# Performance work log

Hardware: AMD Instinct MI355X
Metric: run time of the kernel (lower is better)

Reference implementation:

```python
import jax, jax.numpy as jnp
import numpy as np

N_GENES = 20000
HIDDEN = 64
K_HOPS = 2
N_EDGES = 640000
BATCH = 32
BN_EPS = 1e-5


def setup_inputs() -> dict:
    key = jax.random.key(0)
    ks = jax.random.split(key, 8)
    B, N, d, E = BATCH, N_GENES, HIDDEN, N_EDGES
    x = jax.random.normal(ks[0], (B, N), jnp.float32)
    edge_index = jax.random.randint(ks[1], (2, E), 0, N).astype(jnp.int64)
    gene_emb = jax.random.normal(ks[2], (N, d), jnp.float32) * 0.02
    W_sg = jax.random.normal(ks[3], (d, d), jnp.float32) / np.sqrt(d).astype(np.float32)
    b_sg = jnp.zeros((d,), jnp.float32)
    W1 = jax.random.normal(ks[4], (d, 2 * d), jnp.float32) / np.sqrt(d).astype(np.float32)
    b1 = jnp.zeros((2 * d,), jnp.float32)
    gamma1 = jnp.ones((2 * d,), jnp.float32)
    beta1 = jnp.zeros((2 * d,), jnp.float32)
    W2 = jax.random.normal(ks[5], (2 * d, 1), jnp.float32) / np.sqrt(2 * d).astype(np.float32)
    b2 = jnp.zeros((1,), jnp.float32)
    return dict(x=x, edge_index=edge_index, gene_emb=gene_emb, W_sg=W_sg, b_sg=b_sg,
                W1=W1, b1=b1, gamma1=gamma1, beta1=beta1, W2=W2, b2=b2)


def _sgconv(gene_emb, src, dst, W_sg, b_sg):
    # SGConv: h = (D^{-1/2}(A+I)D^{-1/2})^K X W  on the co-expression graph
    N = gene_emb.shape[0]
    ones = jnp.ones(src.shape, gene_emb.dtype)
    deg = jax.ops.segment_sum(ones, dst, num_segments=N) + 1.0  # +1 self loop
    dinv = jax.lax.rsqrt(deg)
    ew = dinv[src] * dinv[dst]          # [E] symmetric edge norm
    self_w = (dinv * dinv)[:, None]     # [N,1] self-loop weight
    h = gene_emb
    for _ in range(K_HOPS):
        msg = h[src] * ew[:, None]      # gather + scale  [E,d]
        h = jax.ops.segment_sum(msg, dst, num_segments=N) + h * self_w
    return h @ W_sg + b_sg              # [N,d]


def reference(x, edge_index, gene_emb, W_sg, b_sg, W1, b1, gamma1, beta1, W2, b2):
    B, N = x.shape
    src, dst = edge_index[0], edge_index[1]
    h = _sgconv(gene_emb, src, dst, W_sg, b_sg)         # [N,d]
    # per-(cell, gene) state: expression scales the gene's graph embedding
    z = (x[:, :, None] * h[None, :, :]).reshape(B * N, -1)  # [B*N, d]
    # MLP block: Linear -> BatchNorm1d (train-mode batch stats) -> ReLU -> Linear
    z = z @ W1 + b1                                     # [B*N, 2d]
    mu = jnp.mean(z, axis=0)
    var = jnp.var(z, axis=0)
    z = (z - mu) * jax.lax.rsqrt(var + BN_EPS) * gamma1 + beta1
    z = jax.nn.relu(z)
    delta = (z @ W2 + b2).reshape(B, N)                 # per-gene scalar delta
    return x + delta                                    # residual post-perturbation expression
```

## Files before the change

### kernel.cpp

```cpp
#include <hip/hip_runtime.h>
#include <hip/hip_bf16.h>

#define NG 20000
#define HD 64
#define NE 640000
#define NB 32
#define D2 128
#define BN_EPS 1e-5f
#define BSTRIDE 128

__device__ __forceinline__ unsigned pack_bf16(float x, float y) {
    unsigned ux = __float_as_uint(x), uy = __float_as_uint(y);
    unsigned lo = (ux + 0x7FFFu + ((ux >> 16) & 1u)) >> 16;
    unsigned hi = (uy + 0x7FFFu + ((uy >> 16) & 1u)) >> 16;
    return (hi << 16) | lo;
}
__device__ __forceinline__ float2 unpack_bf16(unsigned g) {
    return make_float2(__uint_as_float(g << 16), __uint_as_float(g & 0xFFFF0000u));
}


__global__ void k_scatter(const int* __restrict__ src, const int* __restrict__ dst,
                          int* __restrict__ cnt, int* __restrict__ srcs) {
    int e4 = blockIdx.x * blockDim.x + threadIdx.x;
    int4 s = ((const int4*)src)[e4];
    int4 d = ((const int4*)dst)[e4];
    srcs[(d.x << 7) + atomicAdd(&cnt[d.x], 1)] = s.x;
    srcs[(d.y << 7) + atomicAdd(&cnt[d.y], 1)] = s.y;
    srcs[(d.z << 7) + atomicAdd(&cnt[d.z], 1)] = s.z;
    srcs[(d.w << 7) + atomicAdd(&cnt[d.w], 1)] = s.w;
}

#define MB_COL 79
#define MB_WC  33
#define MB_PRE 625

__global__ __launch_bounds__(256) void k_misc(const float* __restrict__ x,
                                              const float* __restrict__ W_sg,
                                              const float* __restrict__ b_sg,
                                              const float* __restrict__ W1,
                                              const float* __restrict__ emb,
                                              const int* __restrict__ cnt,
                                              float* __restrict__ sx,
                                              float* __restrict__ sxx,
                                              float* __restrict__ S,
                                              float* __restrict__ Wc,
                                              float* __restrict__ bc,
                                              unsigned* __restrict__ g0) {
    int blk = blockIdx.x;
    int tid = threadIdx.x;
    if (blk < MB_COL) {
        if (blk == 0 && tid < 2 * D2) S[tid] = 0.f;
        int n = blk * 256 + tid;
        if (n < NG) {
            float s = 0.f, s2 = 0.f;
            #pragma unroll
            for (int b = 0; b < NB; ++b) {
                float v = x[b * NG + n];
                s += v;
                s2 = fmaf(v, v, s2);
            }
            sx[n] = s;
            sxx[n] = s2;
        }
    } else if (blk < MB_COL + MB_WC) {
        int idx = (blk - MB_COL) * 256 + tid;
        if (idx < HD * D2) {
            int k = idx >> 7, c = idx & (D2 - 1);
            float acc = 0.f;
            #pragma unroll 8
            for (int j = 0; j < HD; ++j) acc += W_sg[k * HD + j] * W1[j * D2 + c];
            Wc[idx] = acc;
        } else if (idx < HD * D2 + D2) {
            int c = idx - HD * D2;
            float acc = 0.f;
            #pragma unroll 8
            for (int j = 0; j < HD; ++j) acc += b_sg[j] * W1[j * D2 + c];
            bc[c] = acc;
        }
    } else {
        int i = (blk - MB_COL - MB_WC) * 256 + tid;
        int row = i >> 3;
        float dv = rsqrtf((float)cnt[row] + 1.0f);
        float4 a = ((const float4*)emb)[i * 2];
        float4 b = ((const float4*)emb)[i * 2 + 1];
        uint4 o;
        o.x = pack_bf16(a.x * dv, a.y * dv);
        o.y = pack_bf16(a.z * dv, a.w * dv);
        o.z = pack_bf16(b.x * dv, b.y * dv);
        o.w = pack_bf16(b.z * dv, b.w * dv);
        ((uint4*)g0)[i] = o;
    }
}

template<bool SQ>
__global__ __launch_bounds__(256) void k_gather(const int* __restrict__ srcs,
                                                const int* __restrict__ cnt,
                                                const unsigned* __restrict__ g,
                                                unsigned* __restrict__ outb,
                                                float4* __restrict__ outf) {
    int n = blockIdx.x * 16 + (threadIdx.x >> 4);
    int l = threadIdx.x & 15;
    const uint2* gp = (const uint2*)g + l;
    int len = cnt[n];
    const int* row = srcs + (n << 7);
    uint2 sv = gp[n * 16];
    float2 a0 = unpack_bf16(sv.x), a1 = unpack_bf16(sv.y);
    float ax = a0.x, ay = a0.y, az = a1.x, aw = a1.y;
    int j = 0;
    for (; j + 3 < len; j += 4) {
        int s0 = row[j], s1 = row[j + 1], s2 = row[j + 2], s3 = row[j + 3];
        uint2 v0 = gp[s0 * 16], v1 = gp[s1 * 16], v2 = gp[s2 * 16], v3 = gp[s3 * 16];
        float2 x0 = unpack_bf16(v0.x), y0 = unpack_bf16(v0.y);
        float2 x1 = unpack_bf16(v1.x), y1 = unpack_bf16(v1.y);
        float2 x2 = unpack_bf16(v2.x), y2 = unpack_bf16(v2.y);
        float2 x3 = unpack_bf16(v3.x), y3 = unpack_bf16(v3.y);
        ax += (x0.x + x1.x) + (x2.x + x3.x);
        ay += (x0.y + x1.y) + (x2.y + x3.y);
        az += (y0.x + y1.x) + (y2.x + y3.x);
        aw += (y0.y + y1.y) + (y2.y + y3.y);
    }
    for (; j < len; ++j) {
        uint2 v0 = gp[row[j] * 16];
        float2 x0 = unpack_bf16(v0.x), y0 = unpack_bf16(v0.y);
        ax += x0.x; ay += x0.y; az += y0.x; aw += y0.y;
    }
    float dv = rsqrtf((float)len + 1.0f);
    float sc = SQ ? dv * dv : dv;
    ax *= sc; ay *= sc; az *= sc; aw *= sc;
    if (SQ) {
        uint2 o;
        o.x = pack_bf16(ax, ay);
        o.y = pack_bf16(az, aw);
        ((uint2*)outb)[n * 16 + l] = o;
    } else {
        outf[n * 16 + l] = make_float4(ax, ay, az, aw);
    }
}

#define PR 32

__global__ __launch_bounds__(256) void k_p_stats(const float* __restrict__ h2,
                                                 const float* __restrict__ Wc,
                                                 const float* __restrict__ bc,
                                                 const float* __restrict__ sx,
                                                 const float* __restrict__ sxx,
                                                 float* __restrict__ p,
                                                 float* __restrict__ S) {
    __shared__ float lWc[HD * D2];
    __shared__ float lt[HD * PR];
    __shared__ float lsx[PR], lsxx[PR];
    int tid = threadIdx.x;
    int n0 = blockIdx.x * PR;

    for (int i = tid; i < HD * D2 / 4; i += 256)
        ((float4*)lWc)[i] = ((const float4*)Wc)[i];
    {
        int r = tid & 31, kb = tid >> 5;
        #pragma unroll
        for (int pp = 0; pp < 2; ++pp) {
            int k4 = kb + pp * 8;
            float4 v = ((const float4*)(h2 + (size_t)(n0 + r) * HD))[k4];
            lt[(k4 * 4 + 0) * PR + r] = v.x;
            lt[(k4 * 4 + 1) * PR + r] = v.y;
            lt[(k4 * 4 + 2) * PR + r] = v.z;
            lt[(k4 * 4 + 3) * PR + r] = v.w;
        }
        if (tid < PR) { lsx[tid] = sx[n0 + tid]; lsxx[tid] = sxx[n0 + tid]; }
    }
    __syncthreads();

    int cg = tid & 31;
    int rg = tid >> 5;
    float acc[4][4];
    #pragma unroll
    for (int i = 0; i < 4; ++i)
        #pragma unroll
        for (int j = 0; j < 4; ++j) acc[i][j] = 0.f;

    #pragma unroll 4
    for (int k = 0; k < HD; ++k) {
        float4 wv = *(const float4*)&lWc[k * D2 + cg * 4];
        float4 hv = *(const float4*)&lt[k * PR + rg * 4];
        acc[0][0] = fmaf(hv.x, wv.x, acc[0][0]);
        acc[0][1] = fmaf(hv.x, wv.y, acc[0][1]);
        acc[0][2] = fmaf(hv.x, wv.z, acc[0][2]);
        acc[0][3] = fmaf(hv.x, wv.w, acc[0][3]);
        acc[1][0] = fmaf(hv.y, wv.x, acc[1][0]);
        acc[1][1] = fmaf(hv.y, wv.y, acc[1][1]);
        acc[1][2] = fmaf(hv.y, wv.z, acc[1][2]);
        acc[1][3] = fmaf(hv.y, wv.w, acc[1][3]);
        acc[2][0] = fmaf(hv.z, wv.x, acc[2][0]);
        acc[2][1] = fmaf(hv.z, wv.y, acc[2][1]);
        acc[2][2] = fmaf(hv.z, wv.z, acc[2][2]);
        acc[2][3] = fmaf(hv.z, wv.w, acc[2][3]);
        acc[3][0] = fmaf(hv.w, wv.x, acc[3][0]);
        acc[3][1] = fmaf(hv.w, wv.y, acc[3][1]);
        acc[3][2] = fmaf(hv.w, wv.z, acc[3][2]);
        acc[3][3] = fmaf(hv.w, wv.w, acc[3][3]);
    }

    float4 bcv = ((const float4*)bc)[cg];
    float s1[4] = {0.f, 0.f, 0.f, 0.f};
    float s2[4] = {0.f, 0.f, 0.f, 0.f};
    #pragma unroll
    for (int i = 0; i < 4; ++i) {
        int rr = rg * 4 + i;
        float xs = lsx[rr], xss = lsxx[rr];
        float4 o;
        o.x = acc[i][0] + bcv.x;
        o.y = acc[i][1] + bcv.y;
        o.z = acc[i][2] + bcv.z;
        o.w = acc[i][3] + bcv.w;
        s1[0] = fmaf(o.x, xs, s1[0]);  s2[0] = fmaf(o.x * o.x, xss, s2[0]);
        s1[1] = fmaf(o.y, xs, s1[1]);  s2[1] = fmaf(o.y * o.y, xss, s2[1]);
        s1[2] = fmaf(o.z, xs, s1[2]);  s2[2] = fmaf(o.z * o.z, xss, s2[2]);
        s1[3] = fmaf(o.w, xs, s1[3]);  s2[3] = fmaf(o.w * o.w, xss, s2[3]);
        ((float4*)(p + (size_t)(n0 + rr) * D2))[cg] = o;
    }

    __syncthreads();
    *(float4*)&lt[rg * D2 + cg * 4]        = make_float4(s1[0], s1[1], s1[2], s1[3]);
    *(float4*)&lt[1024 + rg * D2 + cg * 4] = make_float4(s2[0], s2[1], s2[2], s2[3]);
    __syncthreads();
    if (tid < D2) {
        float a = 0.f, b = 0.f;
        #pragma unroll
        for (int g2 = 0; g2 < 8; ++g2) {
            a += lt[g2 * D2 + tid];
            b += lt[1024 + g2 * D2 + tid];
        }
        atomicAdd(&S[tid], a);
        atomicAdd(&S[D2 + tid], b);
    }
}

#define FN 64

__global__ __launch_bounds__(256) void k_final(const float* __restrict__ x,
                                               const float* __restrict__ p,
                                               const float* __restrict__ S,
                                               const float* __restrict__ gamma1,
                                               const float* __restrict__ beta1,
                                               const float* __restrict__ W2,
                                               const float* __restrict__ b2,
                                               float* __restrict__ out) {
    __shared__ float lp[FN * 129];
    __shared__ float ls[D2], lo[D2], lw[D2];
    int tid = threadIdx.x;
    int n0 = blockIdx.x * FN;
    if (tid < D2) {
        const float inv = 1.0f / (float)(NB * NG);
        float m1 = S[tid] * inv;
        float m2 = S[D2 + tid] * inv;
        float a = gamma1[tid] * rsqrtf(m2 - m1 * m1 + BN_EPS);
        ls[tid] = a;
        lo[tid] = beta1[tid] - m1 * a;
        lw[tid] = W2[tid];
    }
    for (int i = tid; i < FN * D2 / 4; i += 256) {
        int row = i >> 5, c4 = i & 31;
        int n = n0 + row;
        float4 v = (n < NG) ? ((const float4*)(p + n * D2))[c4]
                            : make_float4(0.f, 0.f, 0.f, 0.f);
        float* dp = lp + row * 129 + c4 * 4;
        dp[0] = v.x; dp[1] = v.y; dp[2] = v.z; dp[3] = v.w;
    }
    __syncthreads();
    int nl = tid & 63;
    int n = n0 + nl;
    if (n >= NG) return;
    int bbase = (tid >> 6) * 8;
    const float* prow = lp + nl * 129;
    float b2v = b2[0];
    float xv[8], acc[8];
    #pragma unroll
    for (int bi = 0; bi < 8; ++bi) {
        xv[bi] = x[(bbase + bi) * NG + n];
        acc[bi] = 0.f;
    }
    #pragma unroll 8
    for (int c = 0; c < D2; ++c) {
        float ps = prow[c] * ls[c];
        float ocv = lo[c];
        float wv = lw[c];
        #pragma unroll
        for (int bi = 0; bi < 8; ++bi) {
            float v = fmaxf(fmaf(xv[bi], ps, ocv), 0.f);
            acc[bi] = fmaf(v, wv, acc[bi]);
        }
    }
    #pragma unroll
    for (int bi = 0; bi < 8; ++bi)
        out[(bbase + bi) * NG + n] = xv[bi] + acc[bi] + b2v;
}

extern "C" void kernel_launch(void* const* d_in, const int* in_sizes, int n_in,
                              void* d_out, int out_size, void* d_ws, size_t ws_size,
                              hipStream_t stream) {
    const float* x        = (const float*)d_in[0];
    const int*   ei       = (const int*)d_in[1];
    const float* gene_emb = (const float*)d_in[2];
    const float* W_sg     = (const float*)d_in[3];
    const float* b_sg     = (const float*)d_in[4];
    const float* W1       = (const float*)d_in[5];
    const float* gamma1   = (const float*)d_in[7];
    const float* beta1    = (const float*)d_in[8];
    const float* W2       = (const float*)d_in[9];
    const float* b2       = (const float*)d_in[10];
    float* out = (float*)d_out;

    const int* src = ei;
    const int* dst = ei + NE;

    char* base = (char*)d_ws;
    int*      srcs     = (int*)base;
    int*      cnt      = srcs + NG * BSTRIDE;
    unsigned* g0       = (unsigned*)(cnt + NG);
    unsigned* g1       = g0 + NG * 32;
    float*    h2       = (float*)(g1 + NG * 32);
    float*    Wc       = h2 + NG * HD;
    float*    bc       = Wc + HD * D2;
    float*    p        = bc + D2;
    float*    sx       = p + NG * D2;
    float*    sxx      = sx + NG;
    float*    S        = sxx + NG;

    hipMemsetAsync(cnt, 0, NG * sizeof(int), stream);

    k_scatter<<<NE / 4 / 256, 256, 0, stream>>>(src, dst, cnt, srcs);

    k_misc<<<MB_COL + MB_WC + MB_PRE, 256, 0, stream>>>(x, W_sg, b_sg, W1, gene_emb,
                                                        cnt, sx, sxx, S, Wc, bc, g0);

    k_gather<true><<<NG / 16, 256, 0, stream>>>(srcs, cnt, g0, g1, nullptr);
    k_gather<false><<<NG / 16, 256, 0, stream>>>(srcs, cnt, g1, nullptr, (float4*)h2);

    k_p_stats<<<NG / PR, 256, 0, stream>>>(h2, Wc, bc, sx, sxx, p, S);

    k_final<<<(NG + FN - 1) / FN, 256, 0, stream>>>(x, p, S, gamma1, beta1, W2, b2, out);
}
```

Baseline: 186.6 us.

## Fuse hop-2 gather into projection kernel, use 16-bit neighbor indices and wider gathers

Merges the second aggregation hop into the projection/statistics kernel so h2 is never written to or read back from global memory. Neighbor lists are stored as 16-bit indices, which halves the bucket footprint and lets eight indices load in one vector read. Gathers now move 16-byte rows using 8 lanes per node. The hipMemset is replaced by zeroing inside an init kernel, and the emb prescale step is split into its own launch that runs after the scatter. The 16-bit indices only work because N < 65536, and fewer lanes per node lowers parallelism on each neighbor list.

```diff
diff --git a/kernel.cpp b/kernel.cpp
--- a/kernel.cpp
+++ b/kernel.cpp
@@ -7,7 +7,6 @@
 #define NB 32
 #define D2 128
 #define BN_EPS 1e-5f
-#define BSTRIDE 128
 
 __device__ __forceinline__ unsigned pack_bf16(float x, float y) {
     unsigned ux = __float_as_uint(x), uy = __float_as_uint(y);
@@ -19,39 +18,34 @@
     return make_float2(__uint_as_float(g << 16), __uint_as_float(g & 0xFFFF0000u));
 }
 
-
-__global__ void k_scatter(const int* __restrict__ src, const int* __restrict__ dst,
-                          int* __restrict__ cnt, int* __restrict__ srcs) {
-    int e4 = blockIdx.x * blockDim.x + threadIdx.x;
-    int4 s = ((const int4*)src)[e4];
-    int4 d = ((const int4*)dst)[e4];
-    srcs[(d.x << 7) + atomicAdd(&cnt[d.x], 1)] = s.x;
-    srcs[(d.y << 7) + atomicAdd(&cnt[d.y], 1)] = s.y;
-    srcs[(d.z << 7) + atomicAdd(&cnt[d.z], 1)] = s.z;
-    srcs[(d.w << 7) + atomicAdd(&cnt[d.w], 1)] = s.w;
-}
-
-#define MB_COL 79
-#define MB_WC  33
-#define MB_PRE 625
-
-__global__ __launch_bounds__(256) void k_misc(const float* __restrict__ x,
+__device__ __forceinline__ void acc8(uint4 v, float& a0, float& a1, float& a2, float& a3,
+                                     float& a4, float& a5, float& a6, float& a7) {
+    float2 t0 = unpack_bf16(v.x), t1 = unpack_bf16(v.y);
+    float2 t2 = unpack_bf16(v.z), t3 = unpack_bf16(v.w);
+    a0 += t0.x; a1 += t0.y; a2 += t1.x; a3 += t1.y;
+    a4 += t2.x; a5 += t2.y; a6 += t3.x; a7 += t3.y;
+}
+
+#define IB_ZC 20
+#define IB_S  1
+#define IB_COL 79
+#define IB_WC 33
+
+__global__ __launch_bounds__(256) void k_init(const float* __restrict__ x,
                                               const float* __restrict__ W_sg,
                                               const float* __restrict__ b_sg,
                                               const float* __restrict__ W1,
-                                              const float* __restrict__ emb,
-                                              const int* __restrict__ cnt,
-                                              float* __restrict__ sx,
-                                              float* __restrict__ sxx,
-                                              float* __restrict__ S,
-                                              float* __restrict__ Wc,
-                                              float* __restrict__ bc,
-                                              unsigned* __restrict__ g0) {
-    int blk = blockIdx.x;
-    int tid = threadIdx.x;
-    if (blk < MB_COL) {
-        if (blk == 0 && tid < 2 * D2) S[tid] = 0.f;
-        int n = blk * 256 + tid;
+                                              int* __restrict__ cnt, float* __restrict__ S,
+                                              float* __restrict__ sx, float* __restrict__ sxx,
+                                              float* __restrict__ Wc, float* __restrict__ bc) {
+    int blk = blockIdx.x, tid = threadIdx.x;
+    if (blk < IB_ZC) {
+        int i = blk * 256 + tid;
+        if (i < NG / 4) ((int4*)cnt)[i] = make_int4(0, 0, 0, 0);
+    } else if (blk < IB_ZC + IB_S) {
+        S[tid] = 0.f;
+    } else if (blk < IB_ZC + IB_S + IB_COL) {
+        int n = (blk - IB_ZC - IB_S) * 256 + tid;
         if (n < NG) {
             float s = 0.f, s2 = 0.f;
             #pragma unroll
@@ -63,8 +57,8 @@
             sx[n] = s;
             sxx[n] = s2;
         }
-    } else if (blk < MB_COL + MB_WC) {
-        int idx = (blk - MB_COL) * 256 + tid;
+    } else {
+        int idx = (blk - IB_ZC - IB_S - IB_COL) * 256 + tid;
         if (idx < HD * D2) {
             int k = idx >> 7, c = idx & (D2 - 1);
             float acc = 0.f;
@@ -78,95 +72,151 @@
             for (int j = 0; j < HD; ++j) acc += b_sg[j] * W1[j * D2 + c];
             bc[c] = acc;
         }
-    } else {
-        int i = (blk - MB_COL - MB_WC) * 256 + tid;
-        int row = i >> 3;
-        float dv = rsqrtf((float)cnt[row] + 1.0f);
-        float4 a = ((const float4*)emb)[i * 2];
-        float4 b = ((const float4*)emb)[i * 2 + 1];
-        uint4 o;
-        o.x = pack_bf16(a.x * dv, a.y * dv);
-        o.y = pack_bf16(a.z * dv, a.w * dv);
-        o.z = pack_bf16(b.x * dv, b.y * dv);
-        o.w = pack_bf16(b.z * dv, b.w * dv);
-        ((uint4*)g0)[i] = o;
-    }
-}
-
-template<bool SQ>
-__global__ __launch_bounds__(256) void k_gather(const int* __restrict__ srcs,
+    }
+}
+
+
+__global__ void k_scatter(const int* __restrict__ src, const int* __restrict__ dst,
+                          int* __restrict__ cnt, unsigned short* __restrict__ srcs) {
+    int e4 = blockIdx.x * blockDim.x + threadIdx.x;
+    int4 s = ((const int4*)src)[e4];
+    int4 d = ((const int4*)dst)[e4];
+    srcs[(d.x << 7) + atomicAdd(&cnt[d.x], 1)] = (unsigned short)s.x;
+    srcs[(d.y << 7) + atomicAdd(&cnt[d.y], 1)] = (unsigned short)s.y;
+    srcs[(d.z << 7) + atomicAdd(&cnt[d.z], 1)] = (unsigned short)s.z;
+    srcs[(d.w << 7) + atomicAdd(&cnt[d.w], 1)] = (unsigned short)s.w;
+}
+
+
+__global__ __launch_bounds__(256) void k_pre(const float* __restrict__ emb,
+                                             const int* __restrict__ cnt,
+                                             unsigned* __restrict__ g0) {
+    int i = blockIdx.x * blockDim.x + threadIdx.x;
+    float dv = rsqrtf((float)cnt[i >> 3] + 1.0f);
+    float4 a = ((const float4*)emb)[i * 2];
+    float4 b = ((const float4*)emb)[i * 2 + 1];
+    uint4 o;
+    o.x = pack_bf16(a.x * dv, a.y * dv);
+    o.y = pack_bf16(a.z * dv, a.w * dv);
+    o.z = pack_bf16(b.x * dv, b.y * dv);
+    o.w = pack_bf16(b.z * dv, b.w * dv);
+    ((uint4*)g0)[i] = o;
+}
+
+
+__global__ __launch_bounds__(256) void k_gather1(const unsigned short* __restrict__ srcs,
+                                                 const int* __restrict__ cnt,
+                                                 const unsigned* __restrict__ g,
+                                                 unsigned* __restrict__ outb) {
+    int n = blockIdx.x * 32 + (threadIdx.x >> 3);
+    int l = threadIdx.x & 7;
+    const uint4* gp = (const uint4*)g + l;
+    int len = cnt[n];
+    const unsigned short* row = srcs + ((size_t)n << 7);
+    uint4 sv = gp[(size_t)n * 8];
+    float a0, a1, a2, a3, a4, a5, a6, a7;
+    {
+        float2 t0 = unpack_bf16(sv.x), t1 = unpack_bf16(sv.y);
+        float2 t2 = unpack_bf16(sv.z), t3 = unpack_bf16(sv.w);
+        a0 = t0.x; a1 = t0.y; a2 = t1.x; a3 = t1.y;
+        a4 = t2.x; a5 = t2.y; a6 = t3.x; a7 = t3.y;
+    }
+    int j = 0;
+    for (; j + 8 <= len; j += 8) {
+        uint4 iw = *(const uint4*)(row + j);
+        int i0 = iw.x & 0xFFFF, i1 = iw.x >> 16, i2 = iw.y & 0xFFFF, i3 = iw.y >> 16;
+        int i4 = iw.z & 0xFFFF, i5 = iw.z >> 16, i6 = iw.w & 0xFFFF, i7 = iw.w >> 16;
+        uint4 v0 = gp[(size_t)i0 * 8], v1 = gp[(size_t)i1 * 8];
+        uint4 v2 = gp[(size_t)i2 * 8], v3 = gp[(size_t)i3 * 8];
+        uint4 v4 = gp[(size_t)i4 * 8], v5 = gp[(size_t)i5 * 8];
+        uint4 v6 = gp[(size_t)i6 * 8], v7 = gp[(size_t)i7 * 8];
+        acc8(v0, a0, a1, a2, a3, a4, a5, a6, a7);
+        acc8(v1, a0, a1, a2, a3, a4, a5, a6, a7);
+        acc8(v2, a0, a1, a2, a3, a4, a5, a6, a7);
+        acc8(v3, a0, a1, a2, a3, a4, a5, a6, a7);
+        acc8(v4, a0, a1, a2, a3, a4, a5, a6, a7);
+        acc8(v5, a0, a1, a2, a3, a4, a5, a6, a7);
+        acc8(v6, a0, a1, a2, a3, a4, a5, a6, a7);
+        acc8(v7, a0, a1, a2, a3, a4, a5, a6, a7);
+    }
+    for (; j < len; ++j) {
+        uint4 v = gp[(size_t)row[j] * 8];
+        acc8(v, a0, a1, a2, a3, a4, a5, a6, a7);
+    }
+    float dv = rsqrtf((float)len + 1.0f);
+    float sc = dv * dv;
+    uint4 o;
+    o.x = pack_bf16(a0 * sc, a1 * sc);
+    o.y = pack_bf16(a2 * sc, a3 * sc);
+    o.z = pack_bf16(a4 * sc, a5 * sc);
+    o.w = pack_bf16(a6 * sc, a7 * sc);
+    ((uint4*)outb)[(size_t)n * 8 + l] = o;
+}
+
+
+__global__ __launch_bounds__(256) void k_hop2ps(const unsigned short* __restrict__ srcs,
                                                 const int* __restrict__ cnt,
                                                 const unsigned* __restrict__ g,
-                                                unsigned* __restrict__ outb,
-                                                float4* __restrict__ outf) {
-    int n = blockIdx.x * 16 + (threadIdx.x >> 4);
-    int l = threadIdx.x & 15;
-    const uint2* gp = (const uint2*)g + l;
-    int len = cnt[n];
-    const int* row = srcs + (n << 7);
-    uint2 sv = gp[n * 16];
-    float2 a0 = unpack_bf16(sv.x), a1 = unpack_bf16(sv.y);
-    float ax = a0.x, ay = a0.y, az = a1.x, aw = a1.y;
-    int j = 0;
-    for (; j + 3 < len; j += 4) {
-        int s0 = row[j], s1 = row[j + 1], s2 = row[j + 2], s3 = row[j + 3];
-        uint2 v0 = gp[s0 * 16], v1 = gp[s1 * 16], v2 = gp[s2 * 16], v3 = gp[s3 * 16];
-        float2 x0 = unpack_bf16(v0.x), y0 = unpack_bf16(v0.y);
-        float2 x1 = unpack_bf16(v1.x), y1 = unpack_bf16(v1.y);
-        float2 x2 = unpack_bf16(v2.x), y2 = unpack_bf16(v2.y);
-        float2 x3 = unpack_bf16(v3.x), y3 = unpack_bf16(v3.y);
-        ax += (x0.x + x1.x) + (x2.x + x3.x);
-        ay += (x0.y + x1.y) + (x2.y + x3.y);
-        az += (y0.x + y1.x) + (y2.x + y3.x);
-        aw += (y0.y + y1.y) + (y2.y + y3.y);
-    }
-    for (; j < len; ++j) {
-        uint2 v0 = gp[row[j] * 16];
-        float2 x0 = unpack_bf16(v0.x), y0 = unpack_bf16(v0.y);
-        ax += x0.x; ay += x0.y; az += y0.x; aw += y0.y;
-    }
-    float dv = rsqrtf((float)len + 1.0f);
-    float sc = SQ ? dv * dv : dv;
-    ax *= sc; ay *= sc; az *= sc; aw *= sc;
-    if (SQ) {
-        uint2 o;
-        o.x = pack_bf16(ax, ay);
-        o.y = pack_bf16(az, aw);
-        ((uint2*)outb)[n * 16 + l] = o;
-    } else {
-        outf[n * 16 + l] = make_float4(ax, ay, az, aw);
-    }
-}
-
-#define PR 32
-
-__global__ __launch_bounds__(256) void k_p_stats(const float* __restrict__ h2,
-                                                 const float* __restrict__ Wc,
-                                                 const float* __restrict__ bc,
-                                                 const float* __restrict__ sx,
-                                                 const float* __restrict__ sxx,
-                                                 float* __restrict__ p,
-                                                 float* __restrict__ S) {
+                                                const float* __restrict__ Wc,
+                                                const float* __restrict__ bc,
+                                                const float* __restrict__ sx,
+                                                const float* __restrict__ sxx,
+                                                float* __restrict__ p,
+                                                float* __restrict__ S) {
     __shared__ float lWc[HD * D2];
-    __shared__ float lt[HD * PR];
-    __shared__ float lsx[PR], lsxx[PR];
+    __shared__ float lt[HD * 32];
     int tid = threadIdx.x;
-    int n0 = blockIdx.x * PR;
+    int n0 = blockIdx.x * 32;
 
     for (int i = tid; i < HD * D2 / 4; i += 256)
         ((float4*)lWc)[i] = ((const float4*)Wc)[i];
+
     {
-        int r = tid & 31, kb = tid >> 5;
-        #pragma unroll
-        for (int pp = 0; pp < 2; ++pp) {
-            int k4 = kb + pp * 8;
-            float4 v = ((const float4*)(h2 + (size_t)(n0 + r) * HD))[k4];
-            lt[(k4 * 4 + 0) * PR + r] = v.x;
-            lt[(k4 * 4 + 1) * PR + r] = v.y;
-            lt[(k4 * 4 + 2) * PR + r] = v.z;
-            lt[(k4 * 4 + 3) * PR + r] = v.w;
-        }
-        if (tid < PR) { lsx[tid] = sx[n0 + tid]; lsxx[tid] = sxx[n0 + tid]; }
+        int r = tid >> 3, l = tid & 7;
+        int n = n0 + r;
+        const uint4* gp = (const uint4*)g + l;
+        int len = cnt[n];
+        const unsigned short* row = srcs + ((size_t)n << 7);
+        uint4 sv = gp[(size_t)n * 8];
+        float a0, a1, a2, a3, a4, a5, a6, a7;
+        {
+            float2 t0 = unpack_bf16(sv.x), t1 = unpack_bf16(sv.y);
+            float2 t2 = unpack_bf16(sv.z), t3 = unpack_bf16(sv.w);
+            a0 = t0.x; a1 = t0.y; a2 = t1.x; a3 = t1.y;
+            a4 = t2.x; a5 = t2.y; a6 = t3.x; a7 = t3.y;
+        }
+        int j = 0;
+        for (; j + 8 <= len; j += 8) {
+            uint4 iw = *(const uint4*)(row + j);
+            int i0 = iw.x & 0xFFFF, i1 = iw.x >> 16, i2 = iw.y & 0xFFFF, i3 = iw.y >> 16;
+            int i4 = iw.z & 0xFFFF, i5 = iw.z >> 16, i6 = iw.w & 0xFFFF, i7 = iw.w >> 16;
+            uint4 v0 = gp[(size_t)i0 * 8], v1 = gp[(size_t)i1 * 8];
+            uint4 v2 = gp[(size_t)i2 * 8], v3 = gp[(size_t)i3 * 8];
+            uint4 v4 = gp[(size_t)i4 * 8], v5 = gp[(size_t)i5 * 8];
+            uint4 v6 = gp[(size_t)i6 * 8], v7 = gp[(size_t)i7 * 8];
+            acc8(v0, a0, a1, a2, a3, a4, a5, a6, a7);
+            acc8(v1, a0, a1, a2, a3, a4, a5, a6, a7);
+            acc8(v2, a0, a1, a2, a3, a4, a5, a6, a7);
+            acc8(v3, a0, a1, a2, a3, a4, a5, a6, a7);
+            acc8(v4, a0, a1, a2, a3, a4, a5, a6, a7);
+            acc8(v5, a0, a1, a2, a3, a4, a5, a6, a7);
+            acc8(v6, a0, a1, a2, a3, a4, a5, a6, a7);
+            acc8(v7, a0, a1, a2, a3, a4, a5, a6, a7);
+        }
+        for (; j < len; ++j) {
+            uint4 v = gp[(size_t)row[j] * 8];
+            acc8(v, a0, a1, a2, a3, a4, a5, a6, a7);
+        }
+        float dv = rsqrtf((float)len + 1.0f);
+        int kb = l * 8;
+        lt[(kb + 0) * 32 + r] = a0 * dv;
+        lt[(kb + 1) * 32 + r] = a1 * dv;
+        lt[(kb + 2) * 32 + r] = a2 * dv;
+        lt[(kb + 3) * 32 + r] = a3 * dv;
+        lt[(kb + 4) * 32 + r] = a4 * dv;
+        lt[(kb + 5) * 32 + r] = a5 * dv;
+        lt[(kb + 6) * 32 + r] = a6 * dv;
+        lt[(kb + 7) * 32 + r] = a7 * dv;
     }
     __syncthreads();
 
@@ -181,7 +231,7 @@
     #pragma unroll 4
     for (int k = 0; k < HD; ++k) {
         float4 wv = *(const float4*)&lWc[k * D2 + cg * 4];
-        float4 hv = *(const float4*)&lt[k * PR + rg * 4];
+        float4 hv = *(const float4*)&lt[k * 32 + rg * 4];
         acc[0][0] = fmaf(hv.x, wv.x, acc[0][0]);
         acc[0][1] = fmaf(hv.x, wv.y, acc[0][1]);
         acc[0][2] = fmaf(hv.x, wv.z, acc[0][2]);
@@ -206,7 +256,7 @@
     #pragma unroll
     for (int i = 0; i < 4; ++i) {
         int rr = rg * 4 + i;
-        float xs = lsx[rr], xss = lsxx[rr];
+        float xs = sx[n0 + rr], xss = sxx[n0 + rr];
         float4 o;
         o.x = acc[i][0] + bcv.x;
         o.y = acc[i][1] + bcv.y;
@@ -261,7 +311,7 @@
     for (int i = tid; i < FN * D2 / 4; i += 256) {
         int row = i >> 5, c4 = i & 31;
         int n = n0 + row;
-        float4 v = (n < NG) ? ((const float4*)(p + n * D2))[c4]
+        float4 v = (n < NG) ? ((const float4*)(p + (size_t)n * D2))[c4]
                             : make_float4(0.f, 0.f, 0.f, 0.f);
         float* dp = lp + row * 129 + c4 * 4;
         dp[0] = v.x; dp[1] = v.y; dp[2] = v.z; dp[3] = v.w;
@@ -314,29 +364,24 @@
     const int* dst = ei + NE;
 
     char* base = (char*)d_ws;
-    int*      srcs     = (int*)base;
-    int*      cnt      = srcs + NG * BSTRIDE;
+    unsigned short* srcs = (unsigned short*)base;
+    int*      cnt      = (int*)(base + (size_t)NG * 128 * 2);
     unsigned* g0       = (unsigned*)(cnt + NG);
     unsigned* g1       = g0 + NG * 32;
-    float*    h2       = (float*)(g1 + NG * 32);
-    float*    Wc       = h2 + NG * HD;
+    float*    Wc       = (float*)(g1 + NG * 32);
     float*    bc       = Wc + HD * D2;
     float*    p        = bc + D2;
-    float*    sx       = p + NG * D2;
+    float*    sx       = p + (size_t)NG * D2;
     float*    sxx      = sx + NG;
     float*    S        = sxx + NG;
 
-    hipMemsetAsync(cnt, 0, NG * sizeof(int), stream);
-
+    k_init<<<IB_ZC + IB_S + IB_COL + IB_WC, 256, 0, stream>>>(x, W_sg, b_sg, W1,
+                                                              cnt, S, sx, sxx, Wc, bc);
     k_scatter<<<NE / 4 / 256, 256, 0, stream>>>(src, dst, cnt, srcs);
-
-    k_misc<<<MB_COL + MB_WC + MB_PRE, 256, 0, stream>>>(x, W_sg, b_sg, W1, gene_emb,
-                                                        cnt, sx, sxx, S, Wc, bc, g0);
-
-    k_gather<true><<<NG / 16, 256, 0, stream>>>(srcs, cnt, g0, g1, nullptr);
-    k_gather<false><<<NG / 16, 256, 0, stream>>>(srcs, cnt, g1, nullptr, (float4*)h2);
-
-    k_p_stats<<<NG / PR, 256, 0, stream>>>(h2, Wc, bc, sx, sxx, p, S);
+    k_pre<<<NG * HD / 8 / 256, 256, 0, stream>>>(gene_emb, cnt, g0);
+
+    k_gather1<<<NG / 32, 256, 0, stream>>>(srcs, cnt, g0, g1);
+    k_hop2ps<<<NG / 32, 256, 0, stream>>>(srcs, cnt, g1, Wc, bc, sx, sxx, p, S);
 
     k_final<<<(NG + FN - 1) / FN, 256, 0, stream>>>(x, p, S, gamma1, beta1, W2, b2, out);
 }
```

After: 174.0 us. 6.8% less time.
